# Kernel optimization log

Hardware: AMD Instinct MI355X
Metric: run time of the kernel (lower is better)

The kernel has to match this reference:

```python
import jax, jax.numpy as jnp
import numpy as np

T, N, E = 6, 50000, 1600000
NFEAT, NHID, NCLASS = 256, 256, 16
SLOPE = 11.0 / 48.0  # eval-mode RReLU: mean of default (lower=1/8, upper=1/3)


def _grcu(H_seq, src, dst, val, Wz, Uz, bz, Wr, Ur, br, Wh, Uh, bh, Q0):
    """One GRCU layer: matrix-GRU weight evolution + sparse GCN aggregation per step.
    H_seq: [T, N, in]  src/dst: [T, E] int  val: [T, E]  Q0: [in, out]."""
    n = H_seq.shape[1]

    def step(Q, xs):
        H, s, d, v = xs
        # mat_GRU_cell: x = hidden = prev_Q (z_topk path is unused in this repo's forward)
        z = jax.nn.sigmoid(Wz @ Q + Uz @ Q + bz)
        r = jax.nn.sigmoid(Wr @ Q + Ur @ Q + br)
        h = jnp.tanh(Wh @ Q + Uh @ (r * Q) + bh)
        Qn = (1.0 - z) * Q + z * h
        XW = H @ Qn                                   # [N, out]
        msg = v[:, None] * XW[s]                      # per-edge gather: Ahat row weights
        agg = jax.ops.segment_sum(msg, d, num_segments=n)  # Ahat @ (H @ Qn)
        out = jnp.where(agg >= 0, agg, SLOPE * agg)   # RReLU (eval)
        return Qn, out

    _, out_seq = jax.lax.scan(step, Q0, (H_seq, src, dst, val))
    return out_seq  # [T, N, out]


def setup_inputs() -> dict:
    key = jax.random.key(0)
    ks = iter(jax.random.split(key, 64))

    def rn(shape, scale=0.05):
        return jax.random.normal(next(ks), shape, dtype=jnp.float32) * scale

    inp = {
        "node_feats": jax.random.normal(next(ks), (T, N, NFEAT), dtype=jnp.float32),
        "edge_val": jax.random.uniform(next(ks), (T, E), dtype=jnp.float32),
    }
    for l, (fi, fo) in enumerate([(NFEAT, NHID), (NHID, NHID)]):
        for g in ("z", "r", "h"):
            inp[f"l{l}_W{g}"] = rn((fi, fi))
            inp[f"l{l}_U{g}"] = rn((fi, fi))
            inp[f"l{l}_b{g}"] = jnp.zeros((fi, fo), dtype=jnp.float32)
        inp[f"l{l}_Q0"] = rn((fi, fo))
    inp["mlp_W1"] = rn((NHID, NHID))
    inp["mlp_b1"] = jnp.zeros((NHID,), dtype=jnp.float32)
    inp["mlp_W2"] = rn((NHID, NCLASS))
    inp["mlp_b2"] = jnp.zeros((NCLASS,), dtype=jnp.float32)
    inp["edge_src"] = jax.random.randint(next(ks), (T, E), 0, N, dtype=jnp.int32)
    inp["edge_dst"] = jax.random.randint(next(ks), (T, E), 0, N, dtype=jnp.int32)
    return inp


def reference(node_feats, edge_val,
              l0_Wz, l0_Uz, l0_bz, l0_Wr, l0_Ur, l0_br, l0_Wh, l0_Uh, l0_bh, l0_Q0,
              l1_Wz, l1_Uz, l1_bz, l1_Wr, l1_Ur, l1_br, l1_Wh, l1_Uh, l1_bh, l1_Q0,
              mlp_W1, mlp_b1, mlp_W2, mlp_b2,
              edge_src, edge_dst):
    h1 = _grcu(node_feats, edge_src, edge_dst, edge_val,
               l0_Wz, l0_Uz, l0_bz, l0_Wr, l0_Ur, l0_br, l0_Wh, l0_Uh, l0_bh, l0_Q0)
    h2 = _grcu(h1, edge_src, edge_dst, edge_val,
               l1_Wz, l1_Uz, l1_bz, l1_Wr, l1_Ur, l1_br, l1_Wh, l1_Uh, l1_bh, l1_Q0)
    out = h2[-1]                                    # last timestep, [N, nhid]
    hid = jax.nn.relu(out @ mlp_W1 + mlp_b1)
    logits = hid @ mlp_W2 + mlp_b2
    return jax.nn.log_softmax(logits, axis=1)       # [N, nclass]
```

## Files before the change

kernel.cpp:

```cpp
#include <hip/hip_runtime.h>
#include <cstddef>

#define SLOPE_F (11.0f / 48.0f)

static const int NN = 50000;
static const int EE = 1600000;
static const int D  = 256;
static const int NCH = 196;
static const int GB  = 391;

typedef __attribute__((ext_vector_type(8))) short short8;
typedef __attribute__((ext_vector_type(4))) float f32x4;
typedef __attribute__((ext_vector_type(2))) float f32x2;

__device__ __forceinline__ ushort f2bf(float f) {
    unsigned u = __float_as_uint(f);
    unsigned r = (u + 0x7fffu + ((u >> 16) & 1u)) >> 16;
    return (ushort)r;
}
__device__ __forceinline__ float bf2f(ushort u) {
    return __uint_as_float(((unsigned)u) << 16);
}

__device__ __forceinline__ unsigned enc8(float x) {
    unsigned ux = __float_as_uint(x);
    unsigned sign = (ux >> 31) << 7;
    float ax = __uint_as_float(ux & 0x7fffffffu);
    if (!(ax < 448.f)) return sign | 0x7E;
    if (ax < 0.015625f) {
        int m = (int)(ax * 512.f + 0.5f);
        if (m > 7) return sign | 0x08;
        return sign | m;
    }
    unsigned u = __float_as_uint(ax);
    u += 0x7FFFFu + ((u >> 20) & 1u);
    int e = (int)((u >> 23) & 255) - 127 + 7;
    if (e > 15) return sign | 0x7E;
    return sign | (e << 3) | ((u >> 20) & 7);
}

__global__ __launch_bounds__(256) void prephist_kernel(
        const float* __restrict__ Wz0, const float* __restrict__ Uz0,
        const float* __restrict__ Wr0, const float* __restrict__ Ur0,
        const float* __restrict__ Wh0, const float* __restrict__ Uh0,
        const float* __restrict__ Wz1, const float* __restrict__ Uz1,
        const float* __restrict__ Wr1, const float* __restrict__ Ur1,
        const float* __restrict__ Wh1, const float* __restrict__ Uh1,
        const float* __restrict__ W1,
        ushort* __restrict__ WB, ushort* __restrict__ BtW1,
        const int* __restrict__ dst, int* __restrict__ D4,
        ushort* __restrict__ rank) {
    int b = blockIdx.x;
    int tid = threadIdx.x;
    if (b >= 144) {
        int e = (b - 144) * 256 + tid;
        if (e < EE) {
            int d = dst[e];
            rank[e] = (ushort)atomicAdd(&D4[(e & 3) * NN + d], 1);
        }
        return;
    }
    __shared__ float lt[64][65];
    if (b < 128) {
        int mat = b >> 4;
        int tr = (b >> 2) & 3, tc = b & 3;
        const float* P = nullptr; const float* S = nullptr;
        switch (mat) {
            case 0: P = Wz0; S = Uz0; break;
            case 1: P = Wr0; S = Ur0; break;
            case 2: P = Wh0; break;
            case 3: P = Uh0; break;
            case 4: P = Wz1; S = Uz1; break;
            case 5: P = Wr1; S = Ur1; break;
            case 6: P = Wh1; break;
            default: P = Uh1; break;
        }
#pragma unroll
        for (int r0 = 0; r0 < 64; r0 += 4) {
            int r = r0 + (tid >> 6);
            int c = tid & 63;
            int row = tr * 64 + r, col = tc * 64 + c;
            float v = P[row * 256 + col];
            if (S) v += S[row * 256 + col];
            lt[r][c] = v;
        }
        __syncthreads();
#pragma unroll
        for (int c0 = 0; c0 < 64; c0 += 4) {
            int c = c0 + (tid >> 6);
            int r = tid & 63;
            WB[(size_t)mat * 65536 + (size_t)(tc * 64 + c) * 256 + tr * 64 + r] =
                f2bf(lt[r][c]);
        }
    } else {
        int t = b - 128;
        int tr = (t >> 2) & 3, tc = t & 3;
#pragma unroll
        for (int r0 = 0; r0 < 64; r0 += 4) {
            int r = r0 + (tid >> 6);
            int c = tid & 63;
            lt[r][c] = W1[(tr * 64 + r) * 256 + tc * 64 + c];
        }
        __syncthreads();
#pragma unroll
        for (int c0 = 0; c0 < 64; c0 += 4) {
            int c = c0 + (tid >> 6);
            int r = tid & 63;
            BtW1[(size_t)(tc * 64 + c) * 256 + tr * 64 + r] = f2bf(lt[r][c]);
        }
    }
}

__global__ __launch_bounds__(256) void gruscan_kernel(
        const ushort* __restrict__ WB,
        const float* __restrict__ bz0, const float* __restrict__ br0,
        const float* __restrict__ bh0, const float* __restrict__ Q00,
        const float* __restrict__ bz1, const float* __restrict__ br1,
        const float* __restrict__ bh1, const float* __restrict__ Q01,
        ushort* __restrict__ Bt,
        const int* __restrict__ D4, int* __restrict__ rs, int* __restrict__ base4,
        int* __restrict__ bsum, int* __restrict__ boff, int* __restrict__ done) {
    int tid = threadIdx.x;
    if (blockIdx.x >= 512) {
        __shared__ int wsum[4];
        __shared__ int lastflag;
        int blk = blockIdx.x - 512;
        int i = blk * 256 + tid;
        int lane = tid & 63, wv = tid >> 6;
        int c0 = 0, c1 = 0, c2 = 0, c3 = 0;
        if (i < NN) {
            c0 = D4[i]; c1 = D4[NN + i]; c2 = D4[2 * NN + i]; c3 = D4[3 * NN + i];
        }
        int v = c0 + c1 + c2 + c3;
        int x = v;
#pragma unroll
        for (int off = 1; off < 64; off <<= 1) {
            int t = __shfl_up(x, off, 64);
            if (lane >= off) x += t;
        }
        if (lane == 63) wsum[wv] = x;
        __syncthreads();
        if (tid == 0) {
            int s = 0;
#pragma unroll
            for (int q = 0; q < 4; ++q) { int t = wsum[q]; wsum[q] = s; s += t; }
            bsum[blk] = s;
        }
        __syncthreads();
        if (i < NN) {
            int p = wsum[wv] + x - v;
            rs[i] = p;
            int4 b4;
            b4.x = p; b4.y = p + c0; b4.z = p + c0 + c1; b4.w = p + c0 + c1 + c2;
            *(int4*)&base4[4 * i] = b4;
        }
        __threadfence();
        if (tid == 0) lastflag = (atomicAdd(done, 1) == NCH - 1);
        __syncthreads();
        if (lastflag) {
            __threadfence();
            int bv = (tid < NCH) ? bsum[tid] : 0;
            int bx = bv;
#pragma unroll
            for (int off = 1; off < 64; off <<= 1) {
                int t = __shfl_up(bx, off, 64);
                if (lane >= off) bx += t;
            }
            if (lane == 63) wsum[wv] = bx;
            __syncthreads();
            if (tid == 0) {
                int s = 0;
#pragma unroll
                for (int q = 0; q < 4; ++q) { int t = wsum[q]; wsum[q] = s; s += t; }
            }
            __syncthreads();
            if (tid < NCH) boff[tid] = wsum[wv] + bx - bv;
        }
        return;
    }
    __shared__ float qs[256];
    __shared__ float rqs[256];
    int layer = blockIdx.x >> 8;
    int j = blockIdx.x & 255;
    int i = tid;
    const ushort* Mz = WB + ((size_t)layer * 4 + 0) * 65536;
    const ushort* Mr = WB + ((size_t)layer * 4 + 1) * 65536;
    const ushort* Wh = WB + ((size_t)layer * 4 + 2) * 65536;
    const ushort* Uh = WB + ((size_t)layer * 4 + 3) * 65536;
    const float* bz = layer ? bz1 : bz0;
    const float* br = layer ? br1 : br0;
    const float* bh = layer ? bh1 : bh0;
    const float* Q0 = layer ? Q01 : Q00;

    float bzv = bz[i * 256 + j];
    float brv = br[i * 256 + j];
    float bhv = bh[i * 256 + j];

    qs[i] = Q0[i * 256 + j];
    __syncthreads();

    for (int step = 0; step < 6; ++step) {
        float az = 0.f, ar = 0.f, ah = 0.f;
#pragma unroll 8
        for (int k = 0; k < 256; ++k) {
            float q = qs[k];
            az += bf2f(Mz[k * 256 + i]) * q;
            ar += bf2f(Mr[k * 256 + i]) * q;
            ah += bf2f(Wh[k * 256 + i]) * q;
        }
        float zz = 1.f / (1.f + expf(-(az + bzv)));
        float rr = 1.f / (1.f + expf(-(ar + brv)));
        float qo = qs[i];
        rqs[i] = rr * qo;
        __syncthreads();
        float bu = 0.f;
#pragma unroll 8
        for (int k = 0; k < 256; ++k)
            bu += bf2f(Uh[k * 256 + i]) * rqs[k];
        float h = tanhf(ah + bu + bhv);
        float qn = (1.f - zz) * qo + zz * h;
        __syncthreads();
        qs[i] = qn;
        __syncthreads();
    }
    Bt[(size_t)layer * 65536 + (size_t)j * 256 + i] = f2bf(qs[i]);
}

template <int ASRC, int EPI>
__device__ __forceinline__ void gemm_body(int bid, int tid,
                                          const ushort* __restrict__ A,
                                          const float* __restrict__ Af,
                                          const ushort* __restrict__ Bt,
                                          const float* __restrict__ bias,
                                          unsigned char* __restrict__ C8,
                                          ushort* __restrict__ Cb, int M) {
    int w = tid >> 6, l = tid & 63;
    int lr = l & 15;
    int lk = l >> 4;
    int row0 = bid * 128 + w * 32;
    int ra = row0 + lr;      if (ra > M - 1) ra = M - 1;
    int rb = row0 + 16 + lr; if (rb > M - 1) rb = M - 1;
    const ushort* Ap0  = A  + (size_t)ra * 256 + lk * 8;
    const ushort* Ap1  = A  + (size_t)rb * 256 + lk * 8;
    const float*  Apf0 = Af + (size_t)ra * 256 + lk * 8;
    const float*  Apf1 = Af + (size_t)rb * 256 + lk * 8;
    const ushort* Bp   = Bt + (size_t)lr * 256 + lk * 8;

    f32x4 acc0[16] = {};
    f32x4 acc1[16] = {};
#pragma unroll
    for (int kc = 0; kc < 8; ++kc) {
        short8 a0, a1;
        if (ASRC == 0) {
            a0 = *(const short8*)(Ap0 + kc * 32);
            a1 = *(const short8*)(Ap1 + kc * 32);
        } else {
            float4 f0 = *(const float4*)(Apf0 + kc * 32);
            float4 f1 = *(const float4*)(Apf0 + kc * 32 + 4);
            float4 g0 = *(const float4*)(Apf1 + kc * 32);
            float4 g1 = *(const float4*)(Apf1 + kc * 32 + 4);
            a0[0] = (short)f2bf(f0.x); a0[1] = (short)f2bf(f0.y);
            a0[2] = (short)f2bf(f0.z); a0[3] = (short)f2bf(f0.w);
            a0[4] = (short)f2bf(f1.x); a0[5] = (short)f2bf(f1.y);
            a0[6] = (short)f2bf(f1.z); a0[7] = (short)f2bf(f1.w);
            a1[0] = (short)f2bf(g0.x); a1[1] = (short)f2bf(g0.y);
            a1[2] = (short)f2bf(g0.z); a1[3] = (short)f2bf(g0.w);
            a1[4] = (short)f2bf(g1.x); a1[5] = (short)f2bf(g1.y);
            a1[6] = (short)f2bf(g1.z); a1[7] = (short)f2bf(g1.w);
        }
#pragma unroll
        for (int nb = 0; nb < 16; ++nb) {
            short8 bf = *(const short8*)(Bp + (size_t)nb * 4096 + kc * 32);
            acc0[nb] = __builtin_amdgcn_mfma_f32_16x16x32_bf16(a0, bf, acc0[nb], 0, 0, 0);
            acc1[nb] = __builtin_amdgcn_mfma_f32_16x16x32_bf16(a1, bf, acc1[nb], 0, 0, 0);
        }
    }

    int ro = lk * 4;
    if (EPI == 0) {
#pragma unroll
        for (int q = 0; q < 4; ++q) {
            unsigned w0[4], w1[4];
#pragma unroll
            for (int t = 0; t < 4; ++t) {
                unsigned x0 = 0, x1 = 0;
#pragma unroll
                for (int u = 0; u < 4; ++u) {
                    x0 |= enc8(acc0[t * 4 + u][q]) << (8 * u);
                    x1 |= enc8(acc1[t * 4 + u][q]) << (8 * u);
                }
                w0[t] = x0; w1[t] = x1;
            }
            int g0 = row0 + ro + q;
            if (g0 < M)
                *(uint4*)&C8[(size_t)g0 * 256 + lr * 16] = make_uint4(w0[0], w0[1], w0[2], w0[3]);
            int g1 = row0 + 16 + ro + q;
            if (g1 < M)
                *(uint4*)&C8[(size_t)g1 * 256 + lr * 16] = make_uint4(w1[0], w1[1], w1[2], w1[3]);
        }
    } else {
#pragma unroll
        for (int nb = 0; nb < 16; ++nb) {
            int gc = nb * 16 + lr;
            float bb = bias[gc];
#pragma unroll
            for (int q = 0; q < 4; ++q) {
                int g0 = row0 + ro + q;
                if (g0 < M) Cb[(size_t)g0 * 256 + gc] = f2bf(fmaxf(acc0[nb][q] + bb, 0.f));
                int g1 = row0 + 16 + ro + q;
                if (g1 < M) Cb[(size_t)g1 * 256 + gc] = f2bf(fmaxf(acc1[nb][q] + bb, 0.f));
            }
        }
    }
}

template <int ASRC, int EPI>
__global__ __launch_bounds__(256) void gemm_mfma(const ushort* __restrict__ A,
                                                 const float* __restrict__ Af,
                                                 const ushort* __restrict__ Bt,
                                                 const float* __restrict__ bias,
                                                 unsigned char* __restrict__ C8,
                                                 ushort* __restrict__ Cb, int M) {
    gemm_body<ASRC, EPI>(blockIdx.x, threadIdx.x, A, Af, Bt, bias, C8, Cb, M);
}

__global__ __launch_bounds__(256) void gemsca_kernel(const float* __restrict__ Af,
                                                     const ushort* __restrict__ Bt,
                                                     unsigned char* __restrict__ C8, int M,
                                                     const int* __restrict__ src,
                                                     const int* __restrict__ dst,
                                                     const float* __restrict__ val,
                                                     const int* __restrict__ base4,
                                                     const int* __restrict__ boff,
                                                     const ushort* __restrict__ rank,
                                                     unsigned long long* __restrict__ csr) {
    if (blockIdx.x < GB) {
        gemm_body<1, 0>(blockIdx.x, threadIdx.x, nullptr, Af, Bt, nullptr, C8, nullptr, M);
        return;
    }
    int e = (blockIdx.x - GB) * 256 + threadIdx.x;
    if (e < EE) {
        int d = dst[e];
        int p = base4[4 * d + (e & 3)] + boff[d >> 8] + (int)rank[e];
        unsigned long long pk = (unsigned long long)(unsigned)src[e]
                              | ((unsigned long long)(unsigned)__float_as_uint(val[e]) << 32);
        __builtin_nontemporal_store(pk, &csr[p]);
    }
}

__global__ __launch_bounds__(256) void agg_csr_kernel(const unsigned char* __restrict__ XW,
                                                      const int2* __restrict__ csr,
                                                      const int* __restrict__ rs,
                                                      const int* __restrict__ boff,
                                                      ushort* __restrict__ out) {
    int d = blockIdx.x * 4 + (threadIdx.x >> 6);
    if (d >= NN) return;
    int l = threadIdx.x & 63;
    int h = l >> 5;
    int il = l & 31;
    int beg = rs[d] + boff[d >> 8];
    int end = (d + 1 < NN) ? (rs[d + 1] + boff[(d + 1) >> 8]) : EE;
    float a0 = 0.f, a1 = 0.f, a2 = 0.f, a3 = 0.f;
    float a4 = 0.f, a5 = 0.f, a6 = 0.f, a7 = 0.f;
    int i = beg + h;
    for (; i + 14 < end; i += 16) {
        int2 e[8];
        uint2 x[8];
#pragma unroll
        for (int u = 0; u < 8; ++u) e[u] = csr[i + 2 * u];
#pragma unroll
        for (int u = 0; u < 8; ++u)
            x[u] = *(const uint2*)&XW[(size_t)e[u].x * 256 + il * 8];
#pragma unroll
        for (int u = 0; u < 8; ++u) {
            float v = __int_as_float(e[u].y);
            f32x2 p0 = __builtin_amdgcn_cvt_pk_f32_fp8(x[u].x, false);
            f32x2 p1 = __builtin_amdgcn_cvt_pk_f32_fp8(x[u].x, true);
            f32x2 p2 = __builtin_amdgcn_cvt_pk_f32_fp8(x[u].y, false);
            f32x2 p3 = __builtin_amdgcn_cvt_pk_f32_fp8(x[u].y, true);
            a0 += v * p0.x; a1 += v * p0.y; a2 += v * p1.x; a3 += v * p1.y;
            a4 += v * p2.x; a5 += v * p2.y; a6 += v * p3.x; a7 += v * p3.y;
        }
    }
    for (; i < end; i += 2) {
        int2 e0 = csr[i];
        float v = __int_as_float(e0.y);
        uint2 x0 = *(const uint2*)&XW[(size_t)e0.x * 256 + il * 8];
        f32x2 p0 = __builtin_amdgcn_cvt_pk_f32_fp8(x0.x, false);
        f32x2 p1 = __builtin_amdgcn_cvt_pk_f32_fp8(x0.x, true);
        f32x2 p2 = __builtin_amdgcn_cvt_pk_f32_fp8(x0.y, false);
        f32x2 p3 = __builtin_amdgcn_cvt_pk_f32_fp8(x0.y, true);
        a0 += v * p0.x; a1 += v * p0.y; a2 += v * p1.x; a3 += v * p1.y;
        a4 += v * p2.x; a5 += v * p2.y; a6 += v * p3.x; a7 += v * p3.y;
    }
    a0 += __shfl_xor(a0, 32); a1 += __shfl_xor(a1, 32);
    a2 += __shfl_xor(a2, 32); a3 += __shfl_xor(a3, 32);
    a4 += __shfl_xor(a4, 32); a5 += __shfl_xor(a5, 32);
    a6 += __shfl_xor(a6, 32); a7 += __shfl_xor(a7, 32);
    if (h == 0) {
        float r[8] = {a0, a1, a2, a3, a4, a5, a6, a7};
#pragma unroll
        for (int u = 0; u < 8; ++u) {
            int p = il * 8 + u;
            int c = ((p & 15) << 4) | (p >> 4);
            float v = r[u];
            v = (v >= 0.f) ? v : SLOPE_F * v;
            out[(size_t)d * D + c] = f2bf(v);
        }
    }
}

__global__ void mlp2_kernel(const ushort* __restrict__ hid, const float* __restrict__ W2,
                            const float* __restrict__ b2, float* __restrict__ out, int M) {
    int tid = threadIdx.x;
    int n = blockIdx.x * 16 + (tid >> 4);
    int c = tid & 15;
    if (n >= M) return;
    float acc = b2[c];
    const ushort* hp = hid + (size_t)n * D;
    for (int k = 0; k < D; k += 8) {
        short8 h8 = *(const short8*)(hp + k);
#pragma unroll
        for (int u = 0; u < 8; ++u)
            acc += bf2f((ushort)h8[u]) * W2[(k + u) * 16 + c];
    }
    float m = acc;
#pragma unroll
    for (int off = 1; off < 16; off <<= 1)
        m = fmaxf(m, __shfl_xor(m, off, 16));
    float ex = expf(acc - m);
    float s = ex;
#pragma unroll
    for (int off = 1; off < 16; off <<= 1)
        s += __shfl_xor(s, off, 16);
    out[(size_t)n * 16 + c] = acc - m - logf(s);
}

extern "C" void kernel_launch(void* const* d_in, const int* in_sizes, int n_in,
                              void* d_out, int out_size, void* d_ws, size_t ws_size,
                              hipStream_t stream) {
    const float* node_feats = (const float*)d_in[0];
    const float* edge_val   = (const float*)d_in[1];
    const float* l0_Wz = (const float*)d_in[2];
    const float* l0_Uz = (const float*)d_in[3];
    const float* l0_bz = (const float*)d_in[4];
    const float* l0_Wr = (const float*)d_in[5];
    const float* l0_Ur = (const float*)d_in[6];
    const float* l0_br = (const float*)d_in[7];
    const float* l0_Wh = (const float*)d_in[8];
    const float* l0_Uh = (const float*)d_in[9];
    const float* l0_bh = (const float*)d_in[10];
    const float* l0_Q0 = (const float*)d_in[11];
    const float* l1_Wz = (const float*)d_in[12];
    const float* l1_Uz = (const float*)d_in[13];
    const float* l1_bz = (const float*)d_in[14];
    const float* l1_Wr = (const float*)d_in[15];
    const float* l1_Ur = (const float*)d_in[16];
    const float* l1_br = (const float*)d_in[17];
    const float* l1_Wh = (const float*)d_in[18];
    const float* l1_Uh = (const float*)d_in[19];
    const float* l1_bh = (const float*)d_in[20];
    const float* l1_Q0 = (const float*)d_in[21];
    const float* W1 = (const float*)d_in[22];
    const float* b1 = (const float*)d_in[23];
    const float* W2 = (const float*)d_in[24];
    const float* b2 = (const float*)d_in[25];
    const int* e_src = (const int*)d_in[26];
    const int* e_dst = (const int*)d_in[27];
    float* out = (float*)d_out;

    const size_t BIG = (size_t)NN * D;
    unsigned char* XW8 = (unsigned char*)d_ws;
    ushort* H   = (ushort*)(XW8 + BIG);
    ushort* HID = H + BIG;
    ushort* Bt  = HID + BIG;
    ushort* WB  = Bt + 3 * 65536;
    int2*   csr = (int2*)(WB + 8 * 65536);
    int*    D4  = (int*)(csr + EE);
    int*    done = D4 + 4 * NN;
    int*    rs  = done + 4;
    int*    base4 = rs + NN;
    int*    bsum = base4 + 4 * NN;
    int*    boff = bsum + 200;
    ushort* rank = (ushort*)(boff + 200);

    const float* feats5 = node_feats + (size_t)5 * BIG;
    const int*   src5   = e_src + (size_t)5 * EE;
    const int*   dst5   = e_dst + (size_t)5 * EE;
    const float* val5   = edge_val + (size_t)5 * EE;

    hipMemsetAsync(D4, 0, (4 * NN + 1) * sizeof(int), stream);

    const int histblocks = (EE + 255) / 256;
    prephist_kernel<<<144 + histblocks, 256, 0, stream>>>(
        l0_Wz, l0_Uz, l0_Wr, l0_Ur, l0_Wh, l0_Uh,
        l1_Wz, l1_Uz, l1_Wr, l1_Ur, l1_Wh, l1_Uh,
        W1, WB, Bt + 2 * 65536, dst5, D4, rank);

    gruscan_kernel<<<512 + NCH, 256, 0, stream>>>(WB, l0_bz, l0_br, l0_bh, l0_Q0,
                                                  l1_bz, l1_br, l1_bh, l1_Q0, Bt,
                                                  D4, rs, base4, bsum, boff, done);

    gemsca_kernel<<<GB + histblocks, 256, 0, stream>>>(feats5, Bt + 0 * 65536, XW8, NN,
                                                       src5, dst5, val5, base4, boff,
                                                       rank, (unsigned long long*)csr);

    const int ablocks = (NN + 3) / 4;

    agg_csr_kernel<<<ablocks, 256, 0, stream>>>(XW8, csr, rs, boff, H);

    gemm_mfma<0, 0><<<GB, 256, 0, stream>>>(H, nullptr, Bt + 1 * 65536, nullptr,
                                            XW8, nullptr, NN);
    agg_csr_kernel<<<ablocks, 256, 0, stream>>>(XW8, csr, rs, boff, H);

    gemm_mfma<0, 1><<<GB, 256, 0, stream>>>(H, nullptr, Bt + 2 * 65536, b1,
                                            nullptr, HID, NN);
    mlp2_kernel<<<(NN + 15) / 16, 256, 0, stream>>>(HID, W2, b2, out, NN);
}
```

Baseline: 605.3 us.

## Pack CSR edges into 32 bits with bf16 weights, split histogram eight ways

```diff
diff --git a/kernel.cpp b/kernel.cpp
--- a/kernel.cpp
+++ b/kernel.cpp
@@ -48,7 +48,7 @@
         const float* __restrict__ Wh1, const float* __restrict__ Uh1,
         const float* __restrict__ W1,
         ushort* __restrict__ WB, ushort* __restrict__ BtW1,
-        const int* __restrict__ dst, int* __restrict__ D4,
+        const int* __restrict__ dst, int* __restrict__ D8,
         ushort* __restrict__ rank) {
     int b = blockIdx.x;
     int tid = threadIdx.x;
@@ -56,7 +56,7 @@
         int e = (b - 144) * 256 + tid;
         if (e < EE) {
             int d = dst[e];
-            rank[e] = (ushort)atomicAdd(&D4[(e & 3) * NN + d], 1);
+            rank[e] = (ushort)atomicAdd(&D8[(e & 7) * NN + d], 1);
         }
         return;
     }
@@ -118,7 +118,7 @@
         const float* __restrict__ bz1, const float* __restrict__ br1,
         const float* __restrict__ bh1, const float* __restrict__ Q01,
         ushort* __restrict__ Bt,
-        const int* __restrict__ D4, int* __restrict__ rs, int* __restrict__ base4,
+        const int* __restrict__ D8, int* __restrict__ rs, int* __restrict__ base8,
         int* __restrict__ bsum, int* __restrict__ boff, int* __restrict__ done) {
     int tid = threadIdx.x;
     if (blockIdx.x >= 512) {
@@ -127,11 +127,13 @@
         int blk = blockIdx.x - 512;
         int i = blk * 256 + tid;
         int lane = tid & 63, wv = tid >> 6;
-        int c0 = 0, c1 = 0, c2 = 0, c3 = 0;
-        if (i < NN) {
-            c0 = D4[i]; c1 = D4[NN + i]; c2 = D4[2 * NN + i]; c3 = D4[3 * NN + i];
-        }
-        int v = c0 + c1 + c2 + c3;
+        int c[8];
+        int v = 0;
+#pragma unroll
+        for (int r = 0; r < 8; ++r) {
+            c[r] = (i < NN) ? D8[r * NN + i] : 0;
+            v += c[r];
+        }
         int x = v;
 #pragma unroll
         for (int off = 1; off < 64; off <<= 1) {
@@ -150,9 +152,14 @@
         if (i < NN) {
             int p = wsum[wv] + x - v;
             rs[i] = p;
-            int4 b4;
-            b4.x = p; b4.y = p + c0; b4.z = p + c0 + c1; b4.w = p + c0 + c1 + c2;
-            *(int4*)&base4[4 * i] = b4;
+            int b = p;
+            int4 b0, b1;
+            b0.x = b; b += c[0]; b0.y = b; b += c[1];
+            b0.z = b; b += c[2]; b0.w = b; b += c[3];
+            b1.x = b; b += c[4]; b1.y = b; b += c[5];
+            b1.z = b; b += c[6]; b1.w = b;
+            *(int4*)&base8[8 * i]     = b0;
+            *(int4*)&base8[8 * i + 4] = b1;
         }
         __threadfence();
         if (tid == 0) lastflag = (atomicAdd(done, 1) == NCH - 1);
@@ -330,10 +337,10 @@
                                                      const int* __restrict__ src,
                                                      const int* __restrict__ dst,
                                                      const float* __restrict__ val,
-                                                     const int* __restrict__ base4,
+                                                     const int* __restrict__ base8,
                                                      const int* __restrict__ boff,
                                                      const ushort* __restrict__ rank,
-                                                     unsigned long long* __restrict__ csr) {
+                                                     unsigned* __restrict__ csr) {
     if (blockIdx.x < GB) {
         gemm_body<1, 0>(blockIdx.x, threadIdx.x, nullptr, Af, Bt, nullptr, C8, nullptr, M);
         return;
@@ -341,15 +348,14 @@
     int e = (blockIdx.x - GB) * 256 + threadIdx.x;
     if (e < EE) {
         int d = dst[e];
-        int p = base4[4 * d + (e & 3)] + boff[d >> 8] + (int)rank[e];
-        unsigned long long pk = (unsigned long long)(unsigned)src[e]
-                              | ((unsigned long long)(unsigned)__float_as_uint(val[e]) << 32);
+        int p = base8[8 * d + (e & 7)] + boff[d >> 8] + (int)rank[e];
+        unsigned pk = (unsigned)src[e] | ((unsigned)f2bf(val[e]) << 16);
         __builtin_nontemporal_store(pk, &csr[p]);
     }
 }
 
 __global__ __launch_bounds__(256) void agg_csr_kernel(const unsigned char* __restrict__ XW,
-                                                      const int2* __restrict__ csr,
+                                                      const unsigned* __restrict__ csr,
                                                       const int* __restrict__ rs,
                                                       const int* __restrict__ boff,
                                                       ushort* __restrict__ out) {
@@ -364,16 +370,16 @@
     float a4 = 0.f, a5 = 0.f, a6 = 0.f, a7 = 0.f;
     int i = beg + h;
     for (; i + 14 < end; i += 16) {
-        int2 e[8];
+        unsigned e[8];
         uint2 x[8];
 #pragma unroll
         for (int u = 0; u < 8; ++u) e[u] = csr[i + 2 * u];
 #pragma unroll
         for (int u = 0; u < 8; ++u)
-            x[u] = *(const uint2*)&XW[(size_t)e[u].x * 256 + il * 8];
+            x[u] = *(const uint2*)&XW[(size_t)(e[u] & 0xffffu) * 256 + il * 8];
 #pragma unroll
         for (int u = 0; u < 8; ++u) {
-            float v = __int_as_float(e[u].y);
+            float v = bf2f((ushort)(e[u] >> 16));
             f32x2 p0 = __builtin_amdgcn_cvt_pk_f32_fp8(x[u].x, false);
             f32x2 p1 = __builtin_amdgcn_cvt_pk_f32_fp8(x[u].x, true);
             f32x2 p2 = __builtin_amdgcn_cvt_pk_f32_fp8(x[u].y, false);
@@ -383,9 +389,9 @@
         }
     }
     for (; i < end; i += 2) {
-        int2 e0 = csr[i];
-        float v = __int_as_float(e0.y);
-        uint2 x0 = *(const uint2*)&XW[(size_t)e0.x * 256 + il * 8];
+        unsigned e0 = csr[i];
+        float v = bf2f((ushort)(e0 >> 16));
+        uint2 x0 = *(const uint2*)&XW[(size_t)(e0 & 0xffffu) * 256 + il * 8];
         f32x2 p0 = __builtin_amdgcn_cvt_pk_f32_fp8(x0.x, false);
         f32x2 p1 = __builtin_amdgcn_cvt_pk_f32_fp8(x0.x, true);
         f32x2 p2 = __builtin_amdgcn_cvt_pk_f32_fp8(x0.y, false);
@@ -475,12 +481,12 @@
     ushort* HID = H + BIG;
     ushort* Bt  = HID + BIG;
     ushort* WB  = Bt + 3 * 65536;
-    int2*   csr = (int2*)(WB + 8 * 65536);
-    int*    D4  = (int*)(csr + EE);
-    int*    done = D4 + 4 * NN;
+    unsigned* csr = (unsigned*)(WB + 8 * 65536);
+    int*    D8  = (int*)(csr + EE);
+    int*    done = D8 + 8 * NN;
     int*    rs  = done + 4;
-    int*    base4 = rs + NN;
-    int*    bsum = base4 + 4 * NN;
+    int*    base8 = rs + NN;
+    int*    bsum = base8 + 8 * NN;
     int*    boff = bsum + 200;
     ushort* rank = (ushort*)(boff + 200);
 
@@ -489,21 +495,21 @@
     const int*   dst5   = e_dst + (size_t)5 * EE;
     const float* val5   = edge_val + (size_t)5 * EE;
 
-    hipMemsetAsync(D4, 0, (4 * NN + 1) * sizeof(int), stream);
+    hipMemsetAsync(D8, 0, (8 * NN + 1) * sizeof(int), stream);
 
     const int histblocks = (EE + 255) / 256;
     prephist_kernel<<<144 + histblocks, 256, 0, stream>>>(
         l0_Wz, l0_Uz, l0_Wr, l0_Ur, l0_Wh, l0_Uh,
         l1_Wz, l1_Uz, l1_Wr, l1_Ur, l1_Wh, l1_Uh,
-        W1, WB, Bt + 2 * 65536, dst5, D4, rank);
+        W1, WB, Bt + 2 * 65536, dst5, D8, rank);
 
     gruscan_kernel<<<512 + NCH, 256, 0, stream>>>(WB, l0_bz, l0_br, l0_bh, l0_Q0,
                                                   l1_bz, l1_br, l1_bh, l1_Q0, Bt,
-                                                  D4, rs, base4, bsum, boff, done);
+                                                  D8, rs, base8, bsum, boff, done);
 
     gemsca_kernel<<<GB + histblocks, 256, 0, stream>>>(feats5, Bt + 0 * 65536, XW8, NN,
-                                                       src5, dst5, val5, base4, boff,
-                                                       rank, (unsigned long long*)csr);
+                                                       src5, dst5, val5, base8, boff,
+                                                       rank, csr);
 
     const int ablocks = (NN + 3) / 4;
 
```

After: 592.8 us. -2.1%, faster.
